# Kernel optimization log

Measured on AMD Instinct MI355X. Metric: run time of the kernel, lower is better.

## Reference

```python
import jax, jax.numpy as jnp
import numpy as np

PS = 32
EMBED_DIM = 768
IN_CH = 3
IMG = 1024
NUM_PATCHES = 992  # ini_row = i for H=1024, so need i+32 <= 1024
SPIKE_IDX = np.array([5, 300, 800])
SPIKE_VAL = 1.0e6  # makes val ~= 23.94 < 24 -> nearest size 16 -> subdivided


def _token_layout(iw_np, num_patches, ps, H):
    """Replicates the module's data-dependent patch-size / subpatch-position logic.
    Returns static (rows, cols, sizes) for every output token, in emission order."""
    avg = iw_np.mean()
    val = np.minimum(ps * avg ** 0.05 / iw_np ** 0.05, float(ps))
    choices = np.array([32, 16, 8, 4], dtype=np.float64)  # argmin picks first on tie, like min(list)
    sizes = choices[np.argmin(np.abs(val[:, None] - choices[None, :]), axis=1)].astype(np.int64)
    rows, cols, szs = [], [], []
    for i in range(num_patches):
        ini_col = (i * ps) % H
        ini_row = (i * ps * ps) // H
        s = int(sizes[i])
        if 3 < s < ps:
            ns = ps // s  # num_subpatches; subpatch_size == s
            for j in range(ns):
                rows.append(ini_row + (j * s) // ns)
                cols.append(ini_col + (j * s) % (ns * s))
                szs.append(s)
        else:
            rows.append(ini_row)
            cols.append(ini_col)
            szs.append(ps)
    return np.asarray(rows), np.asarray(cols), np.asarray(szs)


def _embed(x, W, b, rows, cols, szs, ps):
    E, C = W.shape[0], W.shape[1]
    B = x.shape[0]
    T = szs.shape[0]
    out = jnp.zeros((B, T, E), dtype=x.dtype)
    for s in np.unique(szs):
        s = int(s)
        idx = np.nonzero(szs == s)[0]  # static token slots for this size group
        r, c = rows[idx], cols[idx]
        if s == ps:
            Wf = W
        else:
            kd = ps // s  # fold the ps x ps kernel down to s x s, as in the module
            Wf = W.reshape(E, C, kd, kd, s, s).sum(axis=(2, 3))
        ar = np.arange(s)
        # gather [B, C, K, s, s] sub-patches with static advanced indexing
        patches = x[:, :, r[:, None, None] + ar[None, :, None], c[:, None, None] + ar[None, None, :]]
        tok = jnp.einsum('bckhw,echw->bke', patches, Wf) + b  # stride==kernel -> 1 token each
        out = out.at[:, jnp.asarray(idx), :].set(tok)
    return out


def setup_inputs() -> dict:
    key = jax.random.key(0)
    k_x, k_w, k_iw, k_b = jax.random.split(key, 4)
    x = jax.random.normal(k_x, (8, IN_CH, IMG, IMG), dtype=jnp.float32)
    iw = jax.random.uniform(k_iw, (1, NUM_PATCHES), dtype=jnp.float32, minval=0.5, maxval=1.5)
    iw = iw.at[0, SPIKE_IDX].set(SPIKE_VAL)  # 3 high-importance patches -> size-16 subdivision
    W = jax.random.normal(k_w, (EMBED_DIM, IN_CH, PS, PS), dtype=jnp.float32) * 0.02
    b = jax.random.normal(k_b, (EMBED_DIM,), dtype=jnp.float32) * 0.02
    return {"x": x, "importance_weights": iw, "W": W, "b": b, "num_patches": NUM_PATCHES}


def reference(x, importance_weights, W, b, num_patches):
    iw = np.asarray(importance_weights)[0]
    rows, cols, szs = _token_layout(iw, int(num_patches), PS, x.shape[3])
    return _embed(x, W, b, rows, cols, szs, PS)  # [B, T, E]
```

## Files before the change

### kernel.cpp

```cpp
#include <hip/hip_runtime.h>


typedef __attribute__((ext_vector_type(8))) short bf16x8;
typedef __attribute__((ext_vector_type(4))) float f32x4;

#define K_DIM 3072
#define N_DIM 768

__device__ __forceinline__ unsigned short f2bf(float f) {
  unsigned int u = __float_as_uint(f);
  u += 0x7fffu + ((u >> 16) & 1u);
  return (unsigned short)(u >> 16);
}

__device__ __forceinline__ void gload16(const void* g, void* l) {
  __builtin_amdgcn_global_load_lds(
      (const __attribute__((address_space(1))) void*)g,
      (__attribute__((address_space(3))) void*)l, 16, 0, 0);
}

__global__ __launch_bounds__(1024)
void prep_kernel(const float* __restrict__ W, unsigned short* __restrict__ Wb, int w4,
                 const float* __restrict__ iw, int P,
                 int* __restrict__ tokBase, int* __restrict__ tokMask, int NB_W) {
  int bid = blockIdx.x;
  int tid = threadIdx.x;
  if (bid < NB_W) {
    int idx = bid * 1024 + tid;
    if (idx < w4) {
      float4 f = *(const float4*)(W + (size_t)idx * 4);
      ushort4 o;
      o.x = f2bf(f.x); o.y = f2bf(f.y); o.z = f2bf(f.z); o.w = f2bf(f.w);
      *(ushort4*)(Wb + (size_t)idx * 4) = o;
    }
    return;
  }
  __shared__ double s_wsum[16];
  __shared__ double s_avg;
  __shared__ int s_cnt[1024];
  float v = (tid < P) ? iw[tid] : 0.0f;
  double d = (double)v;
#pragma unroll
  for (int off = 32; off > 0; off >>= 1) d += __shfl_down(d, off, 64);
  if ((tid & 63) == 0) s_wsum[tid >> 6] = d;
  __syncthreads();
  if (tid == 0) {
    double s = 0.0;
    for (int i = 0; i < 16; ++i) s += s_wsum[i];
    s_avg = s / (double)P;
  }
  __syncthreads();
  int cnt = 0, sz = 32;
  if (tid < P) {
    double val = 32.0 * pow(s_avg / (double)v, 0.05);
    if (val > 32.0) val = 32.0;
    sz = (val >= 24.0) ? 32 : (val >= 12.0) ? 16 : (val >= 6.0) ? 8 : 4;
    cnt = (sz < 32) ? (32 / sz) : 1;
  }
  s_cnt[tid] = cnt;
  __syncthreads();
  for (int dl = 1; dl < 1024; dl <<= 1) {
    int add = (tid >= dl) ? s_cnt[tid - dl] : 0;
    __syncthreads();
    s_cnt[tid] += add;
    __syncthreads();
  }
  if (tid < P) {
    int off = s_cnt[tid] - cnt;
    int ini_col = (tid * 32) & 1023;
    int ini_row = (tid * 32 * 32) >> 10;
    if (sz == 32) {
      tokBase[off] = ini_row * 1024 + ini_col;
      tokMask[off] = 31;
    } else {
      int ns = 32 / sz;
      for (int j = 0; j < ns; ++j) {
        int r = ini_row + (j * sz) / ns;
        int c = ini_col + ((j * sz) & 31);
        tokBase[off + j] = r * 1024 + c;
        tokMask[off + j] = sz - 1;
      }
    }
  }
}

__global__ __launch_bounds__(256)
void gather_kernel(const float* __restrict__ x,
                   const int* __restrict__ tokBase,
                   const int* __restrict__ tokMask,
                   unsigned short* __restrict__ Ab) {
  int t = blockIdx.x;
  int b = blockIdx.y;
  int T = gridDim.x;
  int m = b * T + t;
  int base = tokBase[t];
  int mask = tokMask[t];
  int sh = __popc(mask);
  const float* xb = x + (size_t)b * 3145728 + (size_t)base;
  unsigned short* arow = Ab + (size_t)m * K_DIM;
#pragma unroll
  for (int it = 0; it < 3; ++it) {
    int g = it * 256 + threadIdx.x;
    int p = g * 4;
    int c = p >> 10;
    int f = p & 1023;
    int h = (f >> sh) & mask;
    int w = f & mask;
    float4 fv = *(const float4*)(xb + (size_t)c * 1048576 + h * 1024 + w);
    ushort4 o;
    o.x = f2bf(fv.x); o.y = f2bf(fv.y); o.z = f2bf(fv.z); o.w = f2bf(fv.w);
    *(ushort4*)(arow + p) = o;
  }
}

__global__ __launch_bounds__(256, 3)
void gemm_kernel(const unsigned short* __restrict__ A, const unsigned short* __restrict__ Wb,
                 const float* __restrict__ bias, float* __restrict__ out, int Mtot) {
  __shared__ unsigned short lds[2][12288];
  int tid = threadIdx.x;
  int lane = tid & 63;
  int wave = tid >> 6;
  int wr = wave >> 1, wc = wave & 1;

  int lin = blockIdx.x;
  int nwg = gridDim.x;
  int q8 = nwg >> 3, r8 = nwg & 7;
  int xcd = lin & 7, slot = lin >> 3;
  int wg = (xcd < r8) ? xcd * (q8 + 1) + slot
                      : r8 * (q8 + 1) + (xcd - r8) * q8 + slot;
  int mBase = (wg / 12) * 128;
  int nBase = (wg % 12) * 64;

  f32x4 acc[4][2] = {};

  int lrow = lane >> 3;
  int schunk = (lane & 7) ^ lrow;
  const unsigned short* Ag = A + (size_t)(mBase + wave * 32 + lrow) * K_DIM + schunk * 8;
  const unsigned short* Bg = Wb + (size_t)(nBase + wave * 16 + lrow) * K_DIM + schunk * 8;
  unsigned short* Adst0 = &lds[0][(wave * 32) * 64] + lane * 8;
  unsigned short* Bdst0 = &lds[0][8192 + (wave * 16) * 64] + lane * 8;

#define STAGE(BUF, KOFF)                                                    \
  {                                                                         \
    _Pragma("unroll")                                                       \
    for (int inst = 0; inst < 4; ++inst)                                    \
      gload16(Ag + (size_t)(inst * 8) * K_DIM + (KOFF),                     \
              Adst0 + (size_t)(BUF) * 12288 + inst * 512);                  \
    _Pragma("unroll")                                                       \
    for (int inst = 0; inst < 2; ++inst)                                    \
      gload16(Bg + (size_t)(inst * 8) * K_DIM + (KOFF),                     \
              Bdst0 + (size_t)(BUF) * 12288 + inst * 512);                  \
  }

  int rr = lane & 15, q = lane >> 4;
  int r7 = rr & 7;

#define COMPUTE(BUF)                                                        \
  {                                                                         \
    const unsigned short* A_ = &lds[BUF][0];                                \
    const unsigned short* B_ = &lds[BUF][8192];                             \
    _Pragma("unroll")                                                       \
    for (int kh = 0; kh < 2; ++kh) {                                        \
      bf16x8 aF[4], bF[2];                                                  \
      _Pragma("unroll")                                                     \
      for (int i = 0; i < 4; ++i)                                           \
        aF[i] = *(const bf16x8*)&A_[(wr * 64 + i * 16 + rr) * 64 +          \
                                    ((kh * 4 + q) ^ r7) * 8];               \
      _Pragma("unroll")                                                     \
      for (int j = 0; j < 2; ++j)                                           \
        bF[j] = *(const bf16x8*)&B_[(wc * 32 + j * 16 + rr) * 64 +          \
                                    ((kh * 4 + q) ^ r7) * 8];               \
      _Pragma("unroll")                                                     \
      for (int i = 0; i < 4; ++i)                                           \
        _Pragma("unroll")                                                   \
        for (int j = 0; j < 2; ++j)                                         \
          acc[i][j] = __builtin_amdgcn_mfma_f32_16x16x32_bf16(aF[i], bF[j], \
                                                              acc[i][j], 0, 0, 0); \
    }                                                                       \
  }

  STAGE(0, 0)
  int buf = 0;
  for (int k0 = 0; k0 < K_DIM - 64; k0 += 64) {
    if (buf == 0) STAGE(1, k0 + 64) else STAGE(0, k0 + 64)
    asm volatile("s_waitcnt vmcnt(6)" ::: "memory");
    __builtin_amdgcn_s_barrier();
    if (buf == 0) COMPUTE(0) else COMPUTE(1)
    asm volatile("s_waitcnt lgkmcnt(0)" ::: "memory");
    __builtin_amdgcn_s_barrier();
    buf ^= 1;
  }
  asm volatile("s_waitcnt vmcnt(0)" ::: "memory");
  __builtin_amdgcn_s_barrier();
  if (buf == 0) COMPUTE(0) else COMPUTE(1)
#undef STAGE
#undef COMPUTE

#pragma unroll
  for (int j = 0; j < 2; ++j) {
    int n = nBase + wc * 32 + j * 16 + rr;
    float bv = bias[n];
#pragma unroll
    for (int i = 0; i < 4; ++i) {
      int mrow = mBase + wr * 64 + i * 16 + q * 4;
#pragma unroll
      for (int r2 = 0; r2 < 4; ++r2) {
        int m = mrow + r2;
        if (m < Mtot) out[(size_t)m * N_DIM + n] = acc[i][j][r2] + bv;
      }
    }
  }
}

extern "C" void kernel_launch(void* const* d_in, const int* in_sizes, int n_in,
                              void* d_out, int out_size, void* d_ws, size_t ws_size,
                              hipStream_t stream) {
  const float* x  = (const float*)d_in[0];
  const float* iw = (const float*)d_in[1];
  const float* W  = (const float*)d_in[2];
  const float* b  = (const float*)d_in[3];
  int P = in_sizes[1];
  int B = in_sizes[0] / (3 * 1024 * 1024);
  int E = in_sizes[3];
  int T = out_size / (B * E);
  int Mtot = B * T;
  int Mpad = (Mtot + 127) & ~127;

  char* ws = (char*)d_ws;
  int* tokBase = (int*)ws;
  int* tokMask = (int*)(ws + 32768);
  unsigned short* Wb = (unsigned short*)(ws + 65536);
  unsigned short* Ab = (unsigned short*)(ws + 65536 + (size_t)E * K_DIM * 2);

  int w4 = E * K_DIM / 4;
  int NB_W = (w4 + 1023) / 1024;
  prep_kernel<<<NB_W + 1, 1024, 0, stream>>>(W, Wb, w4, iw, P, tokBase, tokMask, NB_W);

  dim3 gGrid(T, B);
  gather_kernel<<<gGrid, 256, 0, stream>>>(x, tokBase, tokMask, Ab);


  dim3 grid((N_DIM / 64) * (Mpad / 128));
  gemm_kernel<<<grid, 256, 0, stream>>>(Ab, Wb, b, (float*)d_out, Mtot);
}
```

Baseline: 236.2 us.

## Enlarge GEMM tile to 192x128 with 6 waves and triple-buffered LDS pipeline

Grows the GEMM block tile from 128x64 to 192x128 and uses 384 threads (6 waves) with a 4x4 MFMA accumulator per wave. LDS becomes three buffers, with loads issued two stages ahead under a fully unrolled three-phase loop. Only the first four waves issue global-to-LDS loads. The larger tile raises data reuse per block and cuts the grid to about one wave of blocks across the CUs. In exchange it raises register and LDS pressure and leaves less room to hide latency through occupancy.

```diff
diff --git a/kernel.cpp b/kernel.cpp
--- a/kernel.cpp
+++ b/kernel.cpp
@@ -6,6 +6,8 @@
 
 #define K_DIM 3072
 #define N_DIM 768
+#define BM 192
+#define BN 128
 
 __device__ __forceinline__ unsigned short f2bf(float f) {
   unsigned int u = __float_as_uint(f);
@@ -113,10 +115,10 @@
   }
 }
 
-__global__ __launch_bounds__(256, 3)
+__global__ __launch_bounds__(384)
 void gemm_kernel(const unsigned short* __restrict__ A, const unsigned short* __restrict__ Wb,
                  const float* __restrict__ bias, float* __restrict__ out, int Mtot) {
-  __shared__ unsigned short lds[2][12288];
+  __shared__ unsigned short lds[3][20480];
   int tid = threadIdx.x;
   int lane = tid & 63;
   int wave = tid >> 6;
@@ -128,28 +130,30 @@
   int xcd = lin & 7, slot = lin >> 3;
   int wg = (xcd < r8) ? xcd * (q8 + 1) + slot
                       : r8 * (q8 + 1) + (xcd - r8) * q8 + slot;
-  int mBase = (wg / 12) * 128;
-  int nBase = (wg % 12) * 64;
-
-  f32x4 acc[4][2] = {};
+  int mBase = (wg / 6) * BM;
+  int nBase = (wg % 6) * BN;
+
+  f32x4 acc[4][4] = {};
 
   int lrow = lane >> 3;
   int schunk = (lane & 7) ^ lrow;
-  const unsigned short* Ag = A + (size_t)(mBase + wave * 32 + lrow) * K_DIM + schunk * 8;
-  const unsigned short* Bg = Wb + (size_t)(nBase + wave * 16 + lrow) * K_DIM + schunk * 8;
-  unsigned short* Adst0 = &lds[0][(wave * 32) * 64] + lane * 8;
-  unsigned short* Bdst0 = &lds[0][8192 + (wave * 16) * 64] + lane * 8;
+  const unsigned short* Ag = A + (size_t)(mBase + wave * 48 + lrow) * K_DIM + schunk * 8;
+  const unsigned short* Bg = Wb + (size_t)(nBase + wave * 32 + lrow) * K_DIM + schunk * 8;
+  unsigned short* Adst0 = &lds[0][(wave * 48) * 64] + lane * 8;
+  unsigned short* Bdst0 = &lds[0][12288 + (wave * 32) * 64] + lane * 8;
 
 #define STAGE(BUF, KOFF)                                                    \
   {                                                                         \
-    _Pragma("unroll")                                                       \
-    for (int inst = 0; inst < 4; ++inst)                                    \
-      gload16(Ag + (size_t)(inst * 8) * K_DIM + (KOFF),                     \
-              Adst0 + (size_t)(BUF) * 12288 + inst * 512);                  \
-    _Pragma("unroll")                                                       \
-    for (int inst = 0; inst < 2; ++inst)                                    \
-      gload16(Bg + (size_t)(inst * 8) * K_DIM + (KOFF),                     \
-              Bdst0 + (size_t)(BUF) * 12288 + inst * 512);                  \
+    if (wave < 4) {                                                         \
+      _Pragma("unroll")                                                     \
+      for (int inst = 0; inst < 6; ++inst)                                  \
+        gload16(Ag + (size_t)(inst * 8) * K_DIM + (KOFF),                   \
+                Adst0 + (size_t)(BUF) * 20480 + inst * 512);                \
+      _Pragma("unroll")                                                     \
+      for (int inst = 0; inst < 4; ++inst)                                  \
+        gload16(Bg + (size_t)(inst * 8) * K_DIM + (KOFF),                   \
+                Bdst0 + (size_t)(BUF) * 20480 + inst * 512);                \
+    }                                                                       \
   }
 
   int rr = lane & 15, q = lane >> 4;
@@ -158,47 +162,70 @@
 #define COMPUTE(BUF)                                                        \
   {                                                                         \
     const unsigned short* A_ = &lds[BUF][0];                                \
-    const unsigned short* B_ = &lds[BUF][8192];                             \
+    const unsigned short* B_ = &lds[BUF][12288];                            \
     _Pragma("unroll")                                                       \
     for (int kh = 0; kh < 2; ++kh) {                                        \
-      bf16x8 aF[4], bF[2];                                                  \
+      bf16x8 aF[4], bF[4];                                                  \
       _Pragma("unroll")                                                     \
       for (int i = 0; i < 4; ++i)                                           \
         aF[i] = *(const bf16x8*)&A_[(wr * 64 + i * 16 + rr) * 64 +          \
                                     ((kh * 4 + q) ^ r7) * 8];               \
       _Pragma("unroll")                                                     \
-      for (int j = 0; j < 2; ++j)                                           \
-        bF[j] = *(const bf16x8*)&B_[(wc * 32 + j * 16 + rr) * 64 +          \
+      for (int j = 0; j < 4; ++j)                                           \
+        bF[j] = *(const bf16x8*)&B_[(wc * 64 + j * 16 + rr) * 64 +          \
                                     ((kh * 4 + q) ^ r7) * 8];               \
       _Pragma("unroll")                                                     \
       for (int i = 0; i < 4; ++i)                                           \
         _Pragma("unroll")                                                   \
-        for (int j = 0; j < 2; ++j)                                         \
+        for (int j = 0; j < 4; ++j)                                         \
           acc[i][j] = __builtin_amdgcn_mfma_f32_16x16x32_bf16(aF[i], bF[j], \
                                                               acc[i][j], 0, 0, 0); \
     }                                                                       \
   }
 
   STAGE(0, 0)
-  int buf = 0;
-  for (int k0 = 0; k0 < K_DIM - 64; k0 += 64) {
-    if (buf == 0) STAGE(1, k0 + 64) else STAGE(0, k0 + 64)
-    asm volatile("s_waitcnt vmcnt(6)" ::: "memory");
-    __builtin_amdgcn_s_barrier();
-    if (buf == 0) COMPUTE(0) else COMPUTE(1)
+  STAGE(1, 64)
+  for (int t = 0; t < 15; ++t) {
+    int k = t * 192;
+    STAGE(2, k + 128)
+    asm volatile("s_waitcnt vmcnt(20)" ::: "memory");
+    __builtin_amdgcn_s_barrier();
+    COMPUTE(0)
     asm volatile("s_waitcnt lgkmcnt(0)" ::: "memory");
     __builtin_amdgcn_s_barrier();
-    buf ^= 1;
-  }
+    STAGE(0, k + 192)
+    asm volatile("s_waitcnt vmcnt(20)" ::: "memory");
+    __builtin_amdgcn_s_barrier();
+    COMPUTE(1)
+    asm volatile("s_waitcnt lgkmcnt(0)" ::: "memory");
+    __builtin_amdgcn_s_barrier();
+    STAGE(1, k + 256)
+    asm volatile("s_waitcnt vmcnt(20)" ::: "memory");
+    __builtin_amdgcn_s_barrier();
+    COMPUTE(2)
+    asm volatile("s_waitcnt lgkmcnt(0)" ::: "memory");
+    __builtin_amdgcn_s_barrier();
+  }
+  STAGE(2, 3008)
+  asm volatile("s_waitcnt vmcnt(20)" ::: "memory");
+  __builtin_amdgcn_s_barrier();
+  COMPUTE(0)
+  asm volatile("s_waitcnt lgkmcnt(0)" ::: "memory");
+  __builtin_amdgcn_s_barrier();
+  asm volatile("s_waitcnt vmcnt(10)" ::: "memory");
+  __builtin_amdgcn_s_barrier();
+  COMPUTE(1)
+  asm volatile("s_waitcnt lgkmcnt(0)" ::: "memory");
+  __builtin_amdgcn_s_barrier();
   asm volatile("s_waitcnt vmcnt(0)" ::: "memory");
   __builtin_amdgcn_s_barrier();
-  if (buf == 0) COMPUTE(0) else COMPUTE(1)
+  COMPUTE(2)
 #undef STAGE
 #undef COMPUTE
 
 #pragma unroll
-  for (int j = 0; j < 2; ++j) {
-    int n = nBase + wc * 32 + j * 16 + rr;
+  for (int j = 0; j < 4; ++j) {
+    int n = nBase + wc * 64 + j * 16 + rr;
     float bv = bias[n];
 #pragma unroll
     for (int i = 0; i < 4; ++i) {
@@ -224,7 +251,7 @@
   int E = in_sizes[3];
   int T = out_size / (B * E);
   int Mtot = B * T;
-  int Mpad = (Mtot + 127) & ~127;
+  int mTiles = (Mtot + BM - 1) / BM;
 
   char* ws = (char*)d_ws;
   int* tokBase = (int*)ws;
@@ -240,6 +267,6 @@
   gather_kernel<<<gGrid, 256, 0, stream>>>(x, tokBase, tokMask, Ab);
 
 
-  dim3 grid((N_DIM / 64) * (Mpad / 128));
-  gemm_kernel<<<grid, 256, 0, stream>>>(Ab, Wb, b, (float*)d_out, Mtot);
-}
+  dim3 grid((N_DIM / BN) * mTiles);
+  gemm_kernel<<<grid, 384, 0, stream>>>(Ab, Wb, b, (float*)d_out, Mtot);
+}
```

Measured after the change: 227.1 us. 1.04x faster.
